# Performance work log

Hardware: AMD Instinct MI355X
Metric: run time of the kernel (lower is better)

Reference implementation:

```python
import jax, jax.numpy as jnp
import numpy as np
import math

B, S, D, H = 4, 1024, 2048, 16
DH = D // H          # dim_head = 128
DHID = 128           # dim_hid
DKER = 64            # dim_ker
EPS = 1e-6


def setup_inputs() -> dict:
    key = jax.random.key(0)
    ks = jax.random.split(key, 12)
    a1 = math.sqrt(6.0 / (DH + DHID))
    a2 = math.sqrt(6.0 / (DKER + DHID))
    a3 = math.sqrt(6.0 / (2 * DKER))
    return {
        "q": jax.random.normal(ks[0], (B, S, D), jnp.float32),
        "k": jax.random.normal(ks[1], (B, S, D), jnp.float32),
        "v": jax.random.normal(ks[2], (B, S, D), jnp.float32),
        "lr_attn_mask": jax.random.randint(ks[3], (B, 1, S, S), 0, 2).astype(bool),
        "sparse_norms_lse": jax.random.normal(ks[4], (B, H, S, 1), jnp.float32),
        "sparse_attn_weights": jax.random.normal(ks[5], (B, H, S, S), jnp.float32),
        "kernel_q_mat1": jax.random.uniform(ks[6], (H, DH, DHID), jnp.float32, -a1, a1),
        "kernel_k_mat1": jax.random.uniform(ks[7], (H, DH, DHID), jnp.float32, -a1, a1),
        "kernel_q_mat2": jax.random.uniform(ks[8], (H, DHID, DKER), jnp.float32, -a2, a2),
        "kernel_k_mat2": jax.random.uniform(ks[9], (H, DHID, DKER), jnp.float32, -a2, a2),
        "interaction_k": jax.random.uniform(ks[10], (H, DKER, DKER), jnp.float32, -a3, a3),
        "scalingD": jnp.ones((1, H, 1, DKER), jnp.float32) * 1e-4,
        "scalingD2": jnp.ones((1, H, 1, DKER), jnp.float32) * 1e-4,
        "lambda_constant": 1,
    }


def _gelu(x):
    # torch F.gelu default = exact (erf) gelu
    return jax.nn.gelu(x, approximate=False)


def reference(q, k, v, lr_attn_mask, sparse_norms_lse, sparse_attn_weights,
              kernel_q_mat1, kernel_k_mat1, kernel_q_mat2, kernel_k_mat2,
              interaction_k, scalingD, scalingD2, lambda_constant):
    # split heads: [B,S,D] -> [B,H,S,DH]
    qh = q.reshape(B, S, H, DH).transpose(0, 2, 1, 3)
    kh = k.reshape(B, S, H, DH).transpose(0, 2, 1, 3)
    vh = v.reshape(B, S, H, DH).transpose(0, 2, 1, 3)

    # learned kernel feature maps (dropout=0 -> identity)
    qf = _gelu(jnp.einsum('bhsd,hde->bhse', qh, kernel_q_mat1))
    qf = _gelu(jnp.einsum('bhse,hef->bhsf', qf, kernel_q_mat2))

    kf = _gelu(jnp.einsum('bhsd,hde->bhse', kh, kernel_k_mat1))
    kf = jnp.abs(scalingD) * _gelu(jnp.einsum('bhse,hef->bhsf', kf, kernel_k_mat2))
    kf = kf + jnp.einsum('bhse,hef->bhsf', kf, interaction_k) * scalingD2

    # low-rank (kernelized) scores, masked. [B,H,S,S]
    scores = jnp.einsum('bhse,bhte->bhst', jnp.abs(qf), jnp.abs(kf))
    m = lr_attn_mask.astype(scores.dtype)  # [B,1,S,S] broadcasts
    scores = m * scores

    # log-domain merge with external sparse attention
    lr_norms_lse = jnp.log(scores.sum(axis=-1, keepdims=True) + EPS)
    norm_factor_lse = jnp.logaddexp(lr_norms_lse, sparse_norms_lse)
    logits = jnp.log(scores + EPS) * m + (1.0 - m) * sparse_attn_weights
    attn = jnp.exp(logits - norm_factor_lse)

    out = jnp.einsum('bhst,bhtd->bhsd', attn, vh)
    return out.transpose(0, 2, 1, 3).reshape(B, S, D)
```

## Files before the change

kernel.cpp:

```cpp
#include <hip/hip_runtime.h>


typedef __bf16 bf16_t;
typedef __attribute__((ext_vector_type(8))) __bf16 bf16x8;
typedef __attribute__((ext_vector_type(4))) float f32x4;

#define MFMA(a, b, c) __builtin_amdgcn_mfma_f32_16x16x32_bf16((a), (b), (c), 0, 0, 0)

typedef __attribute__((address_space(3))) void as3_void;
typedef __attribute__((address_space(1))) const void as1_void;
static __device__ __forceinline__ void gload16(const void* g, void* l) {
    __builtin_amdgcn_global_load_lds((as1_void*)g, (as3_void*)l, 16, 0, 0);
}

static __device__ __forceinline__ float gelu_exact(float x) {
    return 0.5f * x * (1.0f + erff(x * 0.70710678118654752f));
}

__global__ __launch_bounds__(256) void conv_weights_kernel(
    const float* __restrict__ wq1, const float* __restrict__ wk1,
    const float* __restrict__ wq2, const float* __restrict__ wk2,
    const float* __restrict__ iK,
    bf16_t* __restrict__ wq1t, bf16_t* __restrict__ wk1t,
    bf16_t* __restrict__ wq2t, bf16_t* __restrict__ wk2t,
    bf16_t* __restrict__ iKt)
{
    const int idx = blockIdx.x * 256 + threadIdx.x;
    if (idx < 16 * 128 * 128) {
        int h = idx >> 14, e = (idx >> 7) & 127, d = idx & 127;
        wq1t[idx] = (bf16_t)wq1[(h << 14) + (d << 7) + e];
        wk1t[idx] = (bf16_t)wk1[(h << 14) + (d << 7) + e];
    }
    if (idx < 16 * 64 * 128) {
        int h = idx >> 13, f = (idx >> 7) & 63, e = idx & 127;
        wq2t[idx] = (bf16_t)wq2[(h << 13) + (e << 6) + f];
        wk2t[idx] = (bf16_t)wk2[(h << 13) + (e << 6) + f];
    }
    if (idx < 16 * 64 * 64) {
        int h = idx >> 12, g = (idx >> 6) & 63, f = idx & 63;
        iKt[idx] = (bf16_t)iK[(h << 12) + (f << 6) + g];
    }
}

__global__ __launch_bounds__(256) void conv_v_kernel(
    const float* __restrict__ v, bf16_t* __restrict__ vT)
{
    __shared__ bf16_t tr[128][72];
    const int bh = blockIdx.x, b = bh >> 4, h = bh & 15;
    const int tt = blockIdx.y;
    const int t0 = tt * 64;
    const int tid = threadIdx.x;
#pragma unroll
    for (int i = 0; i < 8; ++i) {
        int f4 = tid + 256 * i;
        int t = f4 >> 5, c4 = f4 & 31;
        const float4 vv = *reinterpret_cast<const float4*>(
            &v[((size_t)b * 1024 + t0 + t) * 2048 + h * 128 + c4 * 4]);
        tr[c4 * 4 + 0][t] = (bf16_t)vv.x;
        tr[c4 * 4 + 1][t] = (bf16_t)vv.y;
        tr[c4 * 4 + 2][t] = (bf16_t)vv.z;
        tr[c4 * 4 + 3][t] = (bf16_t)vv.w;
    }
    __syncthreads();
#pragma unroll
    for (int i = 0; i < 32; ++i) {
        int e = tid + 256 * i;
        int d = e >> 6, tl = e & 63;
        vT[(((size_t)bh * 16 + tt) * 128 + d) * 64 + tl] = tr[d][tl];
    }
}

__global__ __launch_bounds__(256) void feat_kernel(
    const float* __restrict__ q, const float* __restrict__ k,
    const bf16_t* __restrict__ wq1t, const bf16_t* __restrict__ wq2t,
    const bf16_t* __restrict__ wk1t, const bf16_t* __restrict__ wk2t,
    const bf16_t* __restrict__ iKt,
    const float* __restrict__ sD, const float* __restrict__ sD2,
    bf16_t* __restrict__ qf, bf16_t* __restrict__ kf)
{
    __shared__ bf16_t xa[64][136];
    __shared__ bf16_t h1[64][136];
    __shared__ bf16_t k2[64][72];

    const int tid = threadIdx.x;
    const int lane = tid & 63, w = tid >> 6;
    const int lr = lane & 15, lg = lane >> 4;
    const int row0 = blockIdx.x * 64;
    const int h = blockIdx.y;
    const int path = blockIdx.z;

    const float* X = path ? k : q;
    const bf16_t* w1t = path ? wk1t : wq1t;
    const bf16_t* w2t = path ? wk2t : wq2t;
    bf16_t* outp = path ? kf : qf;

#pragma unroll
    for (int i = 0; i < 8; ++i) {
        int f4 = tid + 256 * i;
        int r = f4 >> 5, c4 = f4 & 31;
        const float4 vv = *reinterpret_cast<const float4*>(
            &X[(size_t)(row0 + r) * 2048 + h * 128 + c4 * 4]);
        xa[r][c4 * 4 + 0] = (bf16_t)vv.x;
        xa[r][c4 * 4 + 1] = (bf16_t)vv.y;
        xa[r][c4 * 4 + 2] = (bf16_t)vv.z;
        xa[r][c4 * 4 + 3] = (bf16_t)vv.w;
    }
    __syncthreads();

    bf16x8 a1[4];
#pragma unroll
    for (int kk = 0; kk < 4; ++kk)
        a1[kk] = *reinterpret_cast<const bf16x8*>(&xa[w * 16 + lr][kk * 32 + lg * 8]);
#pragma unroll
    for (int nt = 0; nt < 8; ++nt) {
        f32x4 acc = {0.f, 0.f, 0.f, 0.f};
#pragma unroll
        for (int kk = 0; kk < 4; ++kk) {
            bf16x8 bfr = *reinterpret_cast<const bf16x8*>(
                &w1t[(size_t)h * 16384 + (nt * 16 + lr) * 128 + kk * 32 + lg * 8]);
            acc = MFMA(a1[kk], bfr, acc);
        }
#pragma unroll
        for (int r = 0; r < 4; ++r)
            h1[w * 16 + lg * 4 + r][nt * 16 + lr] = (bf16_t)gelu_exact(acc[r]);
    }
    __syncthreads();

    bf16x8 a2[4];
#pragma unroll
    for (int kk = 0; kk < 4; ++kk)
        a2[kk] = *reinterpret_cast<const bf16x8*>(&h1[w * 16 + lr][kk * 32 + lg * 8]);

    if (path == 0) {
#pragma unroll
        for (int nt = 0; nt < 4; ++nt) {
            f32x4 acc = {0.f, 0.f, 0.f, 0.f};
#pragma unroll
            for (int kk = 0; kk < 4; ++kk) {
                bf16x8 bfr = *reinterpret_cast<const bf16x8*>(
                    &w2t[(size_t)h * 8192 + (nt * 16 + lr) * 128 + kk * 32 + lg * 8]);
                acc = MFMA(a2[kk], bfr, acc);
            }
#pragma unroll
            for (int r = 0; r < 4; ++r) {
                int n = row0 + w * 16 + lg * 4 + r;
                int bb = n >> 10, s = n & 1023;
                outp[(((size_t)bb * 16 + h) * 1024 + s) * 64 + nt * 16 + lr] =
                    (bf16_t)fabsf(gelu_exact(acc[r]));
            }
        }
    } else {
#pragma unroll
        for (int nt = 0; nt < 4; ++nt) {
            f32x4 acc = {0.f, 0.f, 0.f, 0.f};
#pragma unroll
            for (int kk = 0; kk < 4; ++kk) {
                bf16x8 bfr = *reinterpret_cast<const bf16x8*>(
                    &w2t[(size_t)h * 8192 + (nt * 16 + lr) * 128 + kk * 32 + lg * 8]);
                acc = MFMA(a2[kk], bfr, acc);
            }
#pragma unroll
            for (int r = 0; r < 4; ++r) {
                int f = nt * 16 + lr;
                k2[w * 16 + lg * 4 + r][f] =
                    (bf16_t)(fabsf(sD[h * 64 + f]) * gelu_exact(acc[r]));
            }
        }
        __syncthreads();
        bf16x8 a3[2];
#pragma unroll
        for (int kk = 0; kk < 2; ++kk)
            a3[kk] = *reinterpret_cast<const bf16x8*>(&k2[w * 16 + lr][kk * 32 + lg * 8]);
#pragma unroll
        for (int nt = 0; nt < 4; ++nt) {
            f32x4 acc = {0.f, 0.f, 0.f, 0.f};
#pragma unroll
            for (int kk = 0; kk < 2; ++kk) {
                bf16x8 bfr = *reinterpret_cast<const bf16x8*>(
                    &iKt[(size_t)h * 4096 + (nt * 16 + lr) * 64 + kk * 32 + lg * 8]);
                acc = MFMA(a3[kk], bfr, acc);
            }
#pragma unroll
            for (int r = 0; r < 4; ++r) {
                int row = w * 16 + lg * 4 + r;
                int g = nt * 16 + lr;
                float base = (float)k2[row][g];
                float kv = fabsf(base + acc[r] * sD2[h * 64 + g]);
                int n = row0 + row;
                int bb = n >> 10, s = n & 1023;
                outp[(((size_t)bb * 16 + h) * 1024 + s) * 64 + g] = (bf16_t)kv;
            }
        }
    }
}

__global__ __launch_bounds__(256, 2) void attn_fused_kernel(
    const bf16_t* __restrict__ qf, const bf16_t* __restrict__ kf,
    const bf16_t* __restrict__ vT,
    const unsigned char* __restrict__ mask8,
    const float* __restrict__ saw, const float* __restrict__ lse,
    float* __restrict__ out)
{
    __shared__ bf16_t vbuf[2][128 * 64];
    __shared__ bf16_t ebuf[2][64 * 64];
    __shared__ bf16_t p[64][72];
    __shared__ int mflag;

    const int tid = threadIdx.x;
    const int lane = tid & 63, w = tid >> 6;
    const int lr = lane & 15, lg = lane >> 4;

    const int di = blockIdx.y * 16 + blockIdx.x;
    const int xcd = di & 7, rr = di >> 3;
    const int bh = xcd + 8 * (rr >> 4);
    const int s0 = (rr & 15) * 64;
    const int b = bh >> 4, h = bh & 15;

    if (tid == 0) {
        unsigned a = 0;
        for (int i = 0; i < 64; ++i) a |= mask8[4 * i + 1];
        mflag = (a == 0) ? 1 : 0;
    }
    __syncthreads();
    const bool mask_is_int = (mflag != 0);
    const int* mask32 = (const int*)mask8;

    const int strow = tid >> 2;
    const int stcg = tid & 3;
    const size_t saw_base = ((size_t)bh << 20) + (size_t)(s0 + strow) * 1024 + stcg * 16;
    const size_t m_base   = ((size_t)b << 20) + (size_t)(s0 + strow) * 1024 + stcg * 16;

    const int vrow = tid >> 3;
    const int vcol8 = (tid & 7) ^ (vrow & 7);
    const bf16_t* vt_bh = vT + (size_t)bh * 131072;

    bf16x8 aq0, aq1;
    {
        const size_t qb = ((size_t)bh * 1024 + s0 + w * 16 + lr) * 64;
        aq0 = *reinterpret_cast<const bf16x8*>(&qf[qb + lg * 8]);
        aq1 = *reinterpret_cast<const bf16x8*>(&qf[qb + 32 + lg * 8]);
    }

    const f32x4 fzero = {0.f, 0.f, 0.f, 0.f};
    f32x4 oacc[8];
#pragma unroll
    for (int i = 0; i < 8; ++i) oacc[i] = fzero;
    float rowsum[4] = {0.f, 0.f, 0.f, 0.f};

#define STAGE_VT(BUF, TILE)                                                      \
    {                                                                            \
        const bf16_t* vg = vt_bh + (size_t)(TILE) * 8192 + vcol8 * 8;            \
        char* lb = (char*)&vbuf[BUF][0] + w * 1024;                              \
        _Pragma("unroll")                                                        \
        for (int j = 0; j < 4; ++j)                                              \
            gload16(vg + (size_t)(32 * j + vrow) * 64, lb + j * 4096);           \
    }

    float4 s4[4];
    int4 mi4[4];
    uint4 mu;

#define LOAD_SAWM(TILE)                                                          \
    {                                                                            \
        _Pragma("unroll")                                                        \
        for (int j = 0; j < 4; ++j)                                              \
            s4[j] = *reinterpret_cast<const float4*>(                            \
                &saw[saw_base + (size_t)(TILE) * 64 + j * 4]);                   \
        if (mask_is_int) {                                                       \
            _Pragma("unroll")                                                    \
            for (int j = 0; j < 4; ++j)                                          \
                mi4[j] = *reinterpret_cast<const int4*>(                         \
                    &mask32[m_base + (size_t)(TILE) * 64 + j * 4]);              \
        } else {                                                                 \
            mu = *reinterpret_cast<const uint4*>(                                \
                &mask8[m_base + (size_t)(TILE) * 64]);                           \
        }                                                                        \
    }

#define WRITE_EBUF(BUF)                                                          \
    {                                                                            \
        float srr[16] = {s4[0].x, s4[0].y, s4[0].z, s4[0].w,                     \
                         s4[1].x, s4[1].y, s4[1].z, s4[1].w,                     \
                         s4[2].x, s4[2].y, s4[2].z, s4[2].w,                     \
                         s4[3].x, s4[3].y, s4[3].z, s4[3].w};                    \
        int mrr[16];                                                             \
        if (mask_is_int) {                                                       \
            int t0_[16] = {mi4[0].x, mi4[0].y, mi4[0].z, mi4[0].w,               \
                           mi4[1].x, mi4[1].y, mi4[1].z, mi4[1].w,               \
                           mi4[2].x, mi4[2].y, mi4[2].z, mi4[2].w,               \
                           mi4[3].x, mi4[3].y, mi4[3].z, mi4[3].w};              \
            _Pragma("unroll")                                                    \
            for (int j = 0; j < 16; ++j) mrr[j] = t0_[j];                        \
        } else {                                                                 \
            unsigned ua[4] = {mu.x, mu.y, mu.z, mu.w};                           \
            _Pragma("unroll")                                                    \
            for (int j = 0; j < 16; ++j)                                         \
                mrr[j] = (int)((ua[j >> 2] >> (8 * (j & 3))) & 255u);            \
        }                                                                        \
        bf16x8 e0, e1;                                                           \
        _Pragma("unroll")                                                        \
        for (int j = 0; j < 8; ++j)                                              \
            e0[j] = mrr[j] ? (bf16_t)(-1.0f) : (bf16_t)__expf(srr[j]);           \
        _Pragma("unroll")                                                        \
        for (int j = 0; j < 8; ++j)                                              \
            e1[j] = mrr[8 + j] ? (bf16_t)(-1.0f) : (bf16_t)__expf(srr[8 + j]);   \
        *reinterpret_cast<bf16x8*>(&ebuf[BUF][strow * 64 + stcg * 16]) = e0;     \
        *reinterpret_cast<bf16x8*>(&ebuf[BUF][strow * 64 + stcg * 16 + 8]) = e1; \
    }

    STAGE_VT(0, 0);
    LOAD_SAWM(0);
    WRITE_EBUF(0);
    __syncthreads();

    int cur = 0;
    const int xorv = (lr & 7) << 4;

    for (int i = 0; i < 16; ++i) {
        const int nxt = cur ^ 1;
        const int tnext = (i + 1) & 15;
        STAGE_VT(nxt, tnext);
        LOAD_SAWM(tnext);
        f32x4 c[4];
        {
            const int t0 = i * 64;
#pragma unroll
            for (int nt = 0; nt < 4; ++nt) {
                f32x4 acc = fzero;
                const size_t kb = ((size_t)bh * 1024 + t0 + nt * 16 + lr) * 64;
                bf16x8 kb0 = *reinterpret_cast<const bf16x8*>(&kf[kb + lg * 8]);
                bf16x8 kb1 = *reinterpret_cast<const bf16x8*>(&kf[kb + 32 + lg * 8]);
                acc = MFMA(aq0, kb0, acc);
                acc = MFMA(aq1, kb1, acc);
                c[nt] = acc;
            }
        }
#pragma unroll
        for (int nt = 0; nt < 4; ++nt) {
#pragma unroll
            for (int r = 0; r < 4; ++r) {
                float pe = (float)ebuf[cur][(w * 16 + lg * 4 + r) * 64 + nt * 16 + lr];
                float sc = c[nt][r];
                bool msk = pe < 0.f;
                float wv = msk ? (sc + 1e-6f) : pe;
                rowsum[r] += msk ? sc : 0.f;
                p[w * 16 + lg * 4 + r][nt * 16 + lr] = (bf16_t)wv;
            }
        }
        {
            bf16x8 ap0 = *reinterpret_cast<const bf16x8*>(&p[w * 16 + lr][lg * 8]);
            bf16x8 ap1 = *reinterpret_cast<const bf16x8*>(&p[w * 16 + lr][32 + lg * 8]);
            const char* vb = (const char*)&vbuf[cur][0];
#pragma unroll
            for (int dt = 0; dt < 8; ++dt) {
                const int row = dt * 16 + lr;
                bf16x8 v0 = *reinterpret_cast<const bf16x8*>(
                    vb + row * 128 + ((lg * 16) ^ xorv));
                bf16x8 v1 = *reinterpret_cast<const bf16x8*>(
                    vb + row * 128 + ((64 + lg * 16) ^ xorv));
                oacc[dt] = MFMA(ap0, v0, oacc[dt]);
                oacc[dt] = MFMA(ap1, v1, oacc[dt]);
            }
        }
        WRITE_EBUF(nxt);
        __syncthreads();
        cur = nxt;
    }

#pragma unroll
    for (int r = 0; r < 4; ++r) {
        float s = rowsum[r];
#pragma unroll
        for (int m = 1; m < 16; m <<= 1) s += __shfl_xor(s, m);
        rowsum[r] = s;
    }
    float invden[4];
#pragma unroll
    for (int r = 0; r < 4; ++r) {
        const int srow = s0 + w * 16 + lg * 4 + r;
        invden[r] = 1.0f / (rowsum[r] + 1e-6f + __expf(lse[(size_t)bh * 1024 + srow]));
    }
#pragma unroll
    for (int dt = 0; dt < 8; ++dt) {
#pragma unroll
        for (int r = 0; r < 4; ++r) {
            const int srow = s0 + w * 16 + lg * 4 + r;
            out[((size_t)b * 1024 + srow) * 2048 + h * 128 + dt * 16 + lr] =
                oacc[dt][r] * invden[r];
        }
    }
#undef STAGE_VT
#undef LOAD_SAWM
#undef WRITE_EBUF
}

extern "C" void kernel_launch(void* const* d_in, const int* in_sizes, int n_in,
                              void* d_out, int out_size, void* d_ws, size_t ws_size,
                              hipStream_t stream)
{
    const float* q   = (const float*)d_in[0];
    const float* k   = (const float*)d_in[1];
    const float* v   = (const float*)d_in[2];
    const unsigned char* mask = (const unsigned char*)d_in[3];
    const float* lse = (const float*)d_in[4];
    const float* saw = (const float*)d_in[5];
    const float* wq1 = (const float*)d_in[6];
    const float* wk1 = (const float*)d_in[7];
    const float* wq2 = (const float*)d_in[8];
    const float* wk2 = (const float*)d_in[9];
    const float* iK  = (const float*)d_in[10];
    const float* sD  = (const float*)d_in[11];
    const float* sD2 = (const float*)d_in[12];
    float* out = (float*)d_out;

    bf16_t* wsb  = (bf16_t*)d_ws;
    bf16_t* wq1t = wsb;
    bf16_t* wk1t = wq1t + 262144;
    bf16_t* wq2t = wk1t + 262144;
    bf16_t* wk2t = wq2t + 131072;
    bf16_t* iKt  = wk2t + 131072;
    bf16_t* qf   = iKt  + 65536;
    bf16_t* kf   = qf   + 4194304;
    bf16_t* vT   = kf   + 4194304;

    conv_weights_kernel<<<dim3(1024), dim3(256), 0, stream>>>(
        wq1, wk1, wq2, wk2, iK, wq1t, wk1t, wq2t, wk2t, iKt);
    conv_v_kernel<<<dim3(64, 16), dim3(256), 0, stream>>>(v, vT);
    feat_kernel<<<dim3(64, 16, 2), dim3(256), 0, stream>>>(
        q, k, wq1t, wq2t, wk1t, wk2t, iKt, sD, sD2, qf, kf);
    attn_fused_kernel<<<dim3(16, 64), dim3(256), 0, stream>>>(
        qf, kf, vT, mask, saw, lse, out);
}
```

Baseline: 230.3 us.

## Deepen sparse-weight prefetch, reuse ebuf for P, and raise occupancy to three blocks

```diff
diff --git a/kernel.cpp b/kernel.cpp
--- a/kernel.cpp
+++ b/kernel.cpp
@@ -194,7 +194,7 @@
     }
 }
 
-__global__ __launch_bounds__(256, 2) void attn_fused_kernel(
+__global__ __launch_bounds__(256, 3) void attn_fused_kernel(
     const bf16_t* __restrict__ qf, const bf16_t* __restrict__ kf,
     const bf16_t* __restrict__ vT,
     const unsigned char* __restrict__ mask8,
@@ -202,8 +202,7 @@
     float* __restrict__ out)
 {
     __shared__ bf16_t vbuf[2][128 * 64];
-    __shared__ bf16_t ebuf[2][64 * 64];
-    __shared__ bf16_t p[64][72];
+    __shared__ bf16_t ebuf[2][64 * 72];
     __shared__ int mflag;
 
     const int tid = threadIdx.x;
@@ -225,10 +224,10 @@
     const bool mask_is_int = (mflag != 0);
     const int* mask32 = (const int*)mask8;
 
-    const int strow = tid >> 2;
-    const int stcg = tid & 3;
-    const size_t saw_base = ((size_t)bh << 20) + (size_t)(s0 + strow) * 1024 + stcg * 16;
-    const size_t m_base   = ((size_t)b << 20) + (size_t)(s0 + strow) * 1024 + stcg * 16;
+    const int strow = tid >> 4;
+    const int stcol = (tid & 15) * 4;
+    const size_t saw_base = ((size_t)bh << 20) + (size_t)(s0 + strow) * 1024 + stcol;
+    const size_t m_base   = ((size_t)b << 20) + (size_t)(s0 + strow) * 1024 + stcol;
 
     const int vrow = tid >> 3;
     const int vcol8 = (tid & 7) ^ (vrow & 7);
@@ -256,115 +255,113 @@
             gload16(vg + (size_t)(32 * j + vrow) * 64, lb + j * 4096);           \
     }
 
-    float4 s4[4];
-    int4 mi4[4];
-    uint4 mu;
-
-#define LOAD_SAWM(TILE)                                                          \
+#define LOAD_SAWM(TILE, SS, MI, MU)                                              \
     {                                                                            \
         _Pragma("unroll")                                                        \
         for (int j = 0; j < 4; ++j)                                              \
-            s4[j] = *reinterpret_cast<const float4*>(                            \
-                &saw[saw_base + (size_t)(TILE) * 64 + j * 4]);                   \
+            SS[j] = *reinterpret_cast<const float4*>(                            \
+                &saw[saw_base + (size_t)(TILE) * 64 + (size_t)j * 16384]);       \
         if (mask_is_int) {                                                       \
             _Pragma("unroll")                                                    \
             for (int j = 0; j < 4; ++j)                                          \
-                mi4[j] = *reinterpret_cast<const int4*>(                         \
-                    &mask32[m_base + (size_t)(TILE) * 64 + j * 4]);              \
+                MI[j] = *reinterpret_cast<const int4*>(                          \
+                    &mask32[m_base + (size_t)(TILE) * 64 + (size_t)j * 16384]);  \
         } else {                                                                 \
-            mu = *reinterpret_cast<const uint4*>(                                \
-                &mask8[m_base + (size_t)(TILE) * 64]);                           \
+            _Pragma("unroll")                                                    \
+            for (int j = 0; j < 4; ++j)                                          \
+                MU[j] = *reinterpret_cast<const unsigned*>(                      \
+                    &mask8[m_base + (size_t)(TILE) * 64 + (size_t)j * 16384]);   \
         }                                                                        \
     }
 
-#define WRITE_EBUF(BUF)                                                          \
+#define WRITE_EBUF(BUF, SS, MI, MU)                                              \
     {                                                                            \
-        float srr[16] = {s4[0].x, s4[0].y, s4[0].z, s4[0].w,                     \
-                         s4[1].x, s4[1].y, s4[1].z, s4[1].w,                     \
-                         s4[2].x, s4[2].y, s4[2].z, s4[2].w,                     \
-                         s4[3].x, s4[3].y, s4[3].z, s4[3].w};                    \
-        int mrr[16];                                                             \
-        if (mask_is_int) {                                                       \
-            int t0_[16] = {mi4[0].x, mi4[0].y, mi4[0].z, mi4[0].w,               \
-                           mi4[1].x, mi4[1].y, mi4[1].z, mi4[1].w,               \
-                           mi4[2].x, mi4[2].y, mi4[2].z, mi4[2].w,               \
-                           mi4[3].x, mi4[3].y, mi4[3].z, mi4[3].w};              \
+        _Pragma("unroll")                                                        \
+        for (int j = 0; j < 4; ++j) {                                            \
+            int m0, m1, m2, m3;                                                  \
+            if (mask_is_int) {                                                   \
+                m0 = MI[j].x; m1 = MI[j].y; m2 = MI[j].z; m3 = MI[j].w;          \
+            } else {                                                             \
+                m0 = (int)(MU[j] & 255u);        m1 = (int)((MU[j] >> 8) & 255u);\
+                m2 = (int)((MU[j] >> 16) & 255u); m3 = (int)(MU[j] >> 24);       \
+            }                                                                    \
+            bf16_t e[4];                                                         \
+            e[0] = m0 ? (bf16_t)(-1.0f) : (bf16_t)__expf(SS[j].x);               \
+            e[1] = m1 ? (bf16_t)(-1.0f) : (bf16_t)__expf(SS[j].y);               \
+            e[2] = m2 ? (bf16_t)(-1.0f) : (bf16_t)__expf(SS[j].z);               \
+            e[3] = m3 ? (bf16_t)(-1.0f) : (bf16_t)__expf(SS[j].w);               \
+            *reinterpret_cast<uint2*>(&ebuf[BUF][(strow + 16 * j) * 72 + stcol]) \
+                = *reinterpret_cast<const uint2*>(e);                            \
+        }                                                                        \
+    }
+
+#define PHASE(CUR, T0)                                                           \
+    {                                                                            \
+        f32x4 c[4];                                                              \
+        _Pragma("unroll")                                                        \
+        for (int nt = 0; nt < 4; ++nt) {                                         \
+            f32x4 acc = fzero;                                                   \
+            const size_t kb = ((size_t)bh * 1024 + (T0) + nt * 16 + lr) * 64;    \
+            bf16x8 kb0 = *reinterpret_cast<const bf16x8*>(&kf[kb + lg * 8]);     \
+            bf16x8 kb1 = *reinterpret_cast<const bf16x8*>(&kf[kb + 32 + lg * 8]);\
+            acc = MFMA(aq0, kb0, acc);                                           \
+            acc = MFMA(aq1, kb1, acc);                                           \
+            c[nt] = acc;                                                         \
+        }                                                                        \
+        _Pragma("unroll")                                                        \
+        for (int nt = 0; nt < 4; ++nt) {                                         \
             _Pragma("unroll")                                                    \
-            for (int j = 0; j < 16; ++j) mrr[j] = t0_[j];                        \
-        } else {                                                                 \
-            unsigned ua[4] = {mu.x, mu.y, mu.z, mu.w};                           \
-            _Pragma("unroll")                                                    \
-            for (int j = 0; j < 16; ++j)                                         \
-                mrr[j] = (int)((ua[j >> 2] >> (8 * (j & 3))) & 255u);            \
+            for (int r = 0; r < 4; ++r) {                                        \
+                const int eoff = (w * 16 + lg * 4 + r) * 72 + nt * 16 + lr;      \
+                float pe = (float)ebuf[CUR][eoff];                               \
+                float sc = c[nt][r];                                             \
+                bool msk = pe < 0.f;                                             \
+                float wv = msk ? (sc + 1e-6f) : pe;                              \
+                rowsum[r] += msk ? sc : 0.f;                                     \
+                ebuf[CUR][eoff] = (bf16_t)wv;                                    \
+            }                                                                    \
         }                                                                        \
-        bf16x8 e0, e1;                                                           \
-        _Pragma("unroll")                                                        \
-        for (int j = 0; j < 8; ++j)                                              \
-            e0[j] = mrr[j] ? (bf16_t)(-1.0f) : (bf16_t)__expf(srr[j]);           \
-        _Pragma("unroll")                                                        \
-        for (int j = 0; j < 8; ++j)                                              \
-            e1[j] = mrr[8 + j] ? (bf16_t)(-1.0f) : (bf16_t)__expf(srr[8 + j]);   \
-        *reinterpret_cast<bf16x8*>(&ebuf[BUF][strow * 64 + stcg * 16]) = e0;     \
-        *reinterpret_cast<bf16x8*>(&ebuf[BUF][strow * 64 + stcg * 16 + 8]) = e1; \
-    }
-
+        asm volatile("s_waitcnt lgkmcnt(0)" ::: "memory");                       \
+        __builtin_amdgcn_sched_barrier(0);                                       \
+        bf16x8 ap0 = *reinterpret_cast<const bf16x8*>(                           \
+            &ebuf[CUR][(w * 16 + lr) * 72 + lg * 8]);                            \
+        bf16x8 ap1 = *reinterpret_cast<const bf16x8*>(                           \
+            &ebuf[CUR][(w * 16 + lr) * 72 + 32 + lg * 8]);                       \
+        const char* vb = (const char*)&vbuf[CUR][0];                             \
+        _Pragma("unroll")                                                        \
+        for (int dt = 0; dt < 8; ++dt) {                                         \
+            const int row = dt * 16 + lr;                                        \
+            bf16x8 v0 = *reinterpret_cast<const bf16x8*>(                        \
+                vb + row * 128 + ((lg * 16) ^ xorv));                            \
+            bf16x8 v1 = *reinterpret_cast<const bf16x8*>(                        \
+                vb + row * 128 + ((64 + lg * 16) ^ xorv));                       \
+            oacc[dt] = MFMA(ap0, v0, oacc[dt]);                                  \
+            oacc[dt] = MFMA(ap1, v1, oacc[dt]);                                  \
+        }                                                                        \
+    }
+
+    float4 sawA[4], sawB[4];
+    int4 miA[4], miB[4];
+    unsigned muA[4], muB[4];
+    const int xorv = (lr & 7) << 4;
+
+    LOAD_SAWM(0, sawA, miA, muA);
+    WRITE_EBUF(0, sawA, miA, muA);
+    LOAD_SAWM(1, sawA, miA, muA);
     STAGE_VT(0, 0);
-    LOAD_SAWM(0);
-    WRITE_EBUF(0);
     __syncthreads();
 
-    int cur = 0;
-    const int xorv = (lr & 7) << 4;
-
-    for (int i = 0; i < 16; ++i) {
-        const int nxt = cur ^ 1;
-        const int tnext = (i + 1) & 15;
-        STAGE_VT(nxt, tnext);
-        LOAD_SAWM(tnext);
-        f32x4 c[4];
-        {
-            const int t0 = i * 64;
-#pragma unroll
-            for (int nt = 0; nt < 4; ++nt) {
-                f32x4 acc = fzero;
-                const size_t kb = ((size_t)bh * 1024 + t0 + nt * 16 + lr) * 64;
-                bf16x8 kb0 = *reinterpret_cast<const bf16x8*>(&kf[kb + lg * 8]);
-                bf16x8 kb1 = *reinterpret_cast<const bf16x8*>(&kf[kb + 32 + lg * 8]);
-                acc = MFMA(aq0, kb0, acc);
-                acc = MFMA(aq1, kb1, acc);
-                c[nt] = acc;
-            }
-        }
-#pragma unroll
-        for (int nt = 0; nt < 4; ++nt) {
-#pragma unroll
-            for (int r = 0; r < 4; ++r) {
-                float pe = (float)ebuf[cur][(w * 16 + lg * 4 + r) * 64 + nt * 16 + lr];
-                float sc = c[nt][r];
-                bool msk = pe < 0.f;
-                float wv = msk ? (sc + 1e-6f) : pe;
-                rowsum[r] += msk ? sc : 0.f;
-                p[w * 16 + lg * 4 + r][nt * 16 + lr] = (bf16_t)wv;
-            }
-        }
-        {
-            bf16x8 ap0 = *reinterpret_cast<const bf16x8*>(&p[w * 16 + lr][lg * 8]);
-            bf16x8 ap1 = *reinterpret_cast<const bf16x8*>(&p[w * 16 + lr][32 + lg * 8]);
-            const char* vb = (const char*)&vbuf[cur][0];
-#pragma unroll
-            for (int dt = 0; dt < 8; ++dt) {
-                const int row = dt * 16 + lr;
-                bf16x8 v0 = *reinterpret_cast<const bf16x8*>(
-                    vb + row * 128 + ((lg * 16) ^ xorv));
-                bf16x8 v1 = *reinterpret_cast<const bf16x8*>(
-                    vb + row * 128 + ((64 + lg * 16) ^ xorv));
-                oacc[dt] = MFMA(ap0, v0, oacc[dt]);
-                oacc[dt] = MFMA(ap1, v1, oacc[dt]);
-            }
-        }
-        WRITE_EBUF(nxt);
+    for (int i = 0; i < 16; i += 2) {
+        STAGE_VT(1, i + 1);
+        LOAD_SAWM((i + 2) & 15, sawB, miB, muB);
+        PHASE(0, i * 64);
+        WRITE_EBUF(1, sawA, miA, muA);
         __syncthreads();
-        cur = nxt;
+        STAGE_VT(0, (i + 2) & 15);
+        LOAD_SAWM((i + 3) & 15, sawA, miA, muA);
+        PHASE(1, (i + 1) * 64);
+        WRITE_EBUF(0, sawB, miB, muB);
+        __syncthreads();
     }
 
 #pragma unroll
@@ -392,6 +389,7 @@
 #undef STAGE_VT
 #undef LOAD_SAWM
 #undef WRITE_EBUF
+#undef PHASE
 }
 
 extern "C" void kernel_launch(void* const* d_in, const int* in_sizes, int n_in,
```

New measurement: 301.7 us. +31.0%, slower.
